# Performance work log

Hardware: AMD Instinct MI355X
Metric: run time of the kernel (lower is better)

The kernel has to match this reference:

```python
import jax, jax.numpy as jnp
import numpy as np

B = 16384
S0, S1 = 7, 7
NB, NC = 2, 20
WC, WN = 5.0, 0.5  # weight_coord, weight_noobject
D = NB * 5 + NC  # 30


def setup_inputs() -> dict:
    key = jax.random.key(0)
    k1, k2, k3, k4 = jax.random.split(key, 4)
    predication = jax.random.normal(k1, (B, S0 * S1 * D), dtype=jnp.float32)
    grid = jax.random.randint(k2, (B, S0, S1), 0, 2, dtype=jnp.int32)
    tbox = jax.random.uniform(k3, (B, S0, S1, 4), dtype=jnp.float32)
    # keep target w,h strictly positive (real boxes), offsets in [0,1)
    tbox = tbox.at[..., 2:].set(0.05 + 0.9 * tbox[..., 2:])
    tcls = jax.random.randint(k4, (B, S0, S1), 0, NC, dtype=jnp.int32)
    return {"predication": predication, "grid": grid, "tbox": tbox, "tcls": tcls}


def _yolo_loss(predication, grid, tbox, tcls):
    pred = predication.reshape(B, S0, S1, D)
    conf = jax.nn.sigmoid(pred[..., :NB])                                  # (B,S0,S1,NB)
    pb = jax.nn.sigmoid(pred[..., NB:5 * NB]).reshape(B, S0, S1, NB, 4)    # (B,S0,S1,NB,4)
    cls = jax.nn.softmax(pred[..., 5 * NB:], axis=-1)                      # (B,S0,S1,NC)

    # cell coordinates: x = column index, y = row index (matches the [1,0] swap in torch code)
    xg = jnp.arange(S1, dtype=pred.dtype)[None, None, :]   # (1,1,S1)
    yg = jnp.arange(S0, dtype=pred.dtype)[None, :, None]   # (1,S0,1)

    tox, toy, tw, th = tbox[..., 0], tbox[..., 1], tbox[..., 2], tbox[..., 3]
    tcx = (xg + tox) / S0
    tcy = (yg + toy) / S1

    pcx = (xg[..., None] + pb[..., 0]) / S0   # (B,S0,S1,NB)
    pcy = (yg[..., None] + pb[..., 1]) / S1
    pw, ph = pb[..., 2], pb[..., 3]

    # IOU of each predicted box vs the cell's target box (same formula as _calc_iou)
    tb_ = jnp.minimum(tcx[..., None] + tw[..., None] / 2, pcx + pw / 2) - \
          jnp.maximum(tcx[..., None] - tw[..., None] / 2, pcx - pw / 2)
    lr_ = jnp.minimum(tcy[..., None] + th[..., None] / 2, pcy + ph / 2) - \
          jnp.maximum(tcy[..., None] - th[..., None] / 2, pcy - ph / 2)
    inter = jnp.where((tb_ < 0) | (lr_ < 0), 0.0, tb_ * lr_)
    iou = inter / ((tw * th)[..., None] + pw * ph - inter)                 # (B,S0,S1,NB)

    # best predictor chosen on detached IOUs (original uses pred_boxes.detach())
    best = jnp.argmax(jax.lax.stop_gradient(iou), axis=-1)                 # (B,S0,S1)

    take = lambda a: jnp.take_along_axis(a, best[..., None], axis=-1)[..., 0]
    iou_b = take(iou)          # attached IOU re-used in confidence loss
    conf_b = take(conf)
    pbb = jnp.take_along_axis(pb, best[..., None, None], axis=3)[..., 0, :]  # (B,S0,S1,4)

    cls_t = jnp.take_along_axis(cls, tcls[..., None], axis=-1)[..., 0]

    coord = (pbb[..., 0] - tox) ** 2 + (pbb[..., 1] - toy) ** 2 \
          + (jnp.sqrt(pbb[..., 2]) - jnp.sqrt(tw)) ** 2 \
          + (jnp.sqrt(pbb[..., 3]) - jnp.sqrt(th)) ** 2

    obj_loss = WC * coord + (conf_b - iou_b) ** 2 + (1.0 - cls_t) ** 2     # (B,S0,S1)
    noobj_loss = WN * jnp.sum(conf ** 2, axis=-1)                          # (B,S0,S1)

    objm = (grid == 1).astype(pred.dtype)
    total = jnp.sum(objm * obj_loss + (1.0 - objm) * noobj_loss)
    return total / B


def reference(predication, grid, tbox, tcls):
    return _yolo_loss(predication, grid, tbox, tcls)
```

## Files before the change

### kernel.cpp

```cpp
#include <hip/hip_runtime.h>
#include <math.h>

namespace {

constexpr int kB    = 16384;
constexpr int kS0   = 7;
constexpr int kS1   = 7;
constexpr int kD    = 30;
constexpr int kCells = kB * kS0 * kS1;
constexpr int TPB   = 256;
constexpr int NBLK  = kCells / TPB;
constexpr int NSLOT = 64;
constexpr float kInv7 = 1.0f / 7.0f;
constexpr float kWC = 5.0f;
constexpr float kWN = 0.5f;

__device__ __forceinline__ float sigm(float x) {
    return 1.0f / (1.0f + __expf(-x));
}

__global__ void __launch_bounds__(TPB, 4) yolo_loss_kernel(
    const float* __restrict__ pred,
    const int*   __restrict__ grid,
    const float* __restrict__ tbox,
    const int*   __restrict__ tcls,
    float* __restrict__ partials)
{
    __shared__ float sp[TPB * kD];
    __shared__ float wsum[TPB / 64];

    const int tid   = threadIdx.x;
    const int cell0 = blockIdx.x * TPB;
    const int cell  = cell0 + tid;
    const int wave  = tid >> 6;
    const int lane  = tid & 63;

    const float4* __restrict__ g4 =
        reinterpret_cast<const float4*>(pred + (size_t)cell0 * kD);
    float4* s4 = reinterpret_cast<float4*>(sp);
    const int etid = 1792 + (tid & 127);

    float4 r[8];
    #pragma unroll
    for (int k = 0; k < 7; ++k) r[k] = g4[tid + 256 * k];
    r[7] = g4[etid];

    const float4 tb4 = reinterpret_cast<const float4*>(tbox)[cell];
    const int g  = grid[cell];
    const int tc = tcls[cell];

    __builtin_amdgcn_sched_barrier(0);

    #pragma unroll
    for (int k = 0; k < 7; ++k) s4[tid + 256 * k] = r[k];
    s4[etid] = r[7];
    __syncthreads();

    const int cj = cell % kS1;
    const int ci = (cell / kS1) % kS0;

    float f[kD];
    {
        const float2* p2 = reinterpret_cast<const float2*>(sp + tid * kD);
        #pragma unroll
        for (int q = 0; q < kD / 2; ++q) {
            float2 t = p2[q];
            f[2 * q]     = t.x;
            f[2 * q + 1] = t.y;
        }
    }

    const float tox = tb4.x, toy = tb4.y, tw = tb4.z, th = tb4.w;

    const float conf0 = sigm(f[0]);
    const float conf1 = sigm(f[1]);
    float pbx[2], pby[2], pbw[2], pbh[2];
    #pragma unroll
    for (int k = 0; k < 2; ++k) {
        pbx[k] = sigm(f[2 + 4 * k + 0]);
        pby[k] = sigm(f[2 + 4 * k + 1]);
        pbw[k] = sigm(f[2 + 4 * k + 2]);
        pbh[k] = sigm(f[2 + 4 * k + 3]);
    }

    float cmax = f[10];
    #pragma unroll
    for (int q = 11; q < 30; ++q) cmax = fmaxf(cmax, f[q]);
    float csum = 0.0f, et = 0.0f;
    #pragma unroll
    for (int q = 0; q < 20; ++q) {
        const float e = __expf(f[10 + q] - cmax);
        csum += e;
        et = (q == tc) ? e : et;
    }
    const float cls_t = et / csum;

    const float x = (float)cj, y = (float)ci;
    const float tcx = (x + tox) * kInv7;
    const float tcy = (y + toy) * kInv7;
    const float thw = tw * 0.5f, thh = th * 0.5f;
    const float tarea = tw * th;

    float iou[2];
    #pragma unroll
    for (int k = 0; k < 2; ++k) {
        const float pcx = (x + pbx[k]) * kInv7;
        const float pcy = (y + pby[k]) * kInv7;
        const float pw = pbw[k], ph = pbh[k];
        const float tb_ = fminf(tcx + thw, pcx + pw * 0.5f) - fmaxf(tcx - thw, pcx - pw * 0.5f);
        const float lr_ = fminf(tcy + thh, pcy + ph * 0.5f) - fmaxf(tcy - thh, pcy - ph * 0.5f);
        float inter = tb_ * lr_;
        inter = (tb_ < 0.0f || lr_ < 0.0f) ? 0.0f : inter;
        iou[k] = inter / (tarea + pw * ph - inter);
    }

    const bool b1 = (iou[1] > iou[0]);
    const float bx = b1 ? pbx[1] : pbx[0];
    const float by = b1 ? pby[1] : pby[0];
    const float bw = b1 ? pbw[1] : pbw[0];
    const float bh = b1 ? pbh[1] : pbh[0];
    const float conf_b = b1 ? conf1 : conf0;
    const float iou_b  = b1 ? iou[1] : iou[0];

    const float dx = bx - tox;
    const float dy = by - toy;
    const float dw = sqrtf(bw) - sqrtf(tw);
    const float dh = sqrtf(bh) - sqrtf(th);
    const float coord = dx * dx + dy * dy + dw * dw + dh * dh;
    const float d1 = conf_b - iou_b;
    const float d2 = 1.0f - cls_t;
    const float obj   = kWC * coord + d1 * d1 + d2 * d2;
    const float noobj = kWN * (conf0 * conf0 + conf1 * conf1);

    float v = (g == 1) ? obj : noobj;

    #pragma unroll
    for (int off = 32; off > 0; off >>= 1) v += __shfl_down(v, off, 64);
    if (lane == 0) wsum[wave] = v;
    __syncthreads();
    if (tid == 0) {
        atomicAdd(&partials[blockIdx.x & (NSLOT - 1)],
                  wsum[0] + wsum[1] + wsum[2] + wsum[3]);
    }
}

__global__ void finish_kernel(const float* __restrict__ partials,
                              float* __restrict__ out)
{
    float v = partials[threadIdx.x];
    #pragma unroll
    for (int off = 32; off > 0; off >>= 1) v += __shfl_down(v, off, 64);
    if (threadIdx.x == 0) out[0] = v * (1.0f / kB);
}

}

extern "C" void kernel_launch(void* const* d_in, const int* in_sizes, int n_in,
                              void* d_out, int out_size, void* d_ws, size_t ws_size,
                              hipStream_t stream) {
    const float* pred = (const float*)d_in[0];
    const int*   grid = (const int*)d_in[1];
    const float* tbox = (const float*)d_in[2];
    const int*   tcls = (const int*)d_in[3];
    float* out      = (float*)d_out;
    float* partials = (float*)d_ws;

    hipMemsetAsync(partials, 0, NSLOT * sizeof(float), stream);
    yolo_loss_kernel<<<NBLK, TPB, 0, stream>>>(pred, grid, tbox, tcls, partials);
    finish_kernel<<<1, 64, 0, stream>>>(partials, out);
}
```

Measured before the change: 160.4 us.

## Drop memset and atomics, use fast reciprocals, skip softmax max-subtraction

Each block now writes its partial sum to its own slot, so the memset launch and the atomics go away; the finish kernel then reduces all per-block partials with 256 threads. Divisions are replaced by the hardware reciprocal, and the softmax max-subtraction is removed. A scheduling barrier is added after the shared-memory loads. Dropping the max-subtraction risks exp overflow on large logits, and the reciprocal lowers precision. The finish kernel now has to read many partials serially per thread.

```diff
diff --git a/kernel.cpp b/kernel.cpp
--- a/kernel.cpp
+++ b/kernel.cpp
@@ -10,13 +10,16 @@
 constexpr int kCells = kB * kS0 * kS1;
 constexpr int TPB   = 256;
 constexpr int NBLK  = kCells / TPB;
-constexpr int NSLOT = 64;
 constexpr float kInv7 = 1.0f / 7.0f;
 constexpr float kWC = 5.0f;
 constexpr float kWN = 0.5f;
 
+__device__ __forceinline__ float frcp(float x) {
+    return __builtin_amdgcn_rcpf(x);
+}
+
 __device__ __forceinline__ float sigm(float x) {
-    return 1.0f / (1.0f + __expf(-x));
+    return frcp(1.0f + __expf(-x));
 }
 
 __global__ void __launch_bounds__(TPB, 4) yolo_loss_kernel(
@@ -68,6 +71,7 @@
             f[2 * q]     = t.x;
             f[2 * q + 1] = t.y;
         }
+        __builtin_amdgcn_sched_barrier(0);
     }
 
     const float tox = tb4.x, toy = tb4.y, tw = tb4.z, th = tb4.w;
@@ -83,17 +87,14 @@
         pbh[k] = sigm(f[2 + 4 * k + 3]);
     }
 
-    float cmax = f[10];
-    #pragma unroll
-    for (int q = 11; q < 30; ++q) cmax = fmaxf(cmax, f[q]);
     float csum = 0.0f, et = 0.0f;
     #pragma unroll
     for (int q = 0; q < 20; ++q) {
-        const float e = __expf(f[10 + q] - cmax);
+        const float e = __expf(f[10 + q]);
         csum += e;
         et = (q == tc) ? e : et;
     }
-    const float cls_t = et / csum;
+    const float cls_t = et * frcp(csum);
 
     const float x = (float)cj, y = (float)ci;
     const float tcx = (x + tox) * kInv7;
@@ -111,7 +112,7 @@
         const float lr_ = fminf(tcy + thh, pcy + ph * 0.5f) - fmaxf(tcy - thh, pcy - ph * 0.5f);
         float inter = tb_ * lr_;
         inter = (tb_ < 0.0f || lr_ < 0.0f) ? 0.0f : inter;
-        iou[k] = inter / (tarea + pw * ph - inter);
+        iou[k] = inter * frcp(tarea + pw * ph - inter);
     }
 
     const bool b1 = (iou[1] > iou[0]);
@@ -139,18 +140,22 @@
     if (lane == 0) wsum[wave] = v;
     __syncthreads();
     if (tid == 0) {
-        atomicAdd(&partials[blockIdx.x & (NSLOT - 1)],
-                  wsum[0] + wsum[1] + wsum[2] + wsum[3]);
+        partials[blockIdx.x] = wsum[0] + wsum[1] + wsum[2] + wsum[3];
     }
 }
 
-__global__ void finish_kernel(const float* __restrict__ partials,
-                              float* __restrict__ out)
+__global__ void __launch_bounds__(256) finish_kernel(
+    const float* __restrict__ partials, float* __restrict__ out)
 {
-    float v = partials[threadIdx.x];
+    __shared__ float wsum[4];
+    const int tid = threadIdx.x;
+    float v = 0.0f;
+    for (int i = tid; i < NBLK; i += 256) v += partials[i];
     #pragma unroll
     for (int off = 32; off > 0; off >>= 1) v += __shfl_down(v, off, 64);
-    if (threadIdx.x == 0) out[0] = v * (1.0f / kB);
+    if ((tid & 63) == 0) wsum[tid >> 6] = v;
+    __syncthreads();
+    if (tid == 0) out[0] = (wsum[0] + wsum[1] + wsum[2] + wsum[3]) * (1.0f / kB);
 }
 
 }
@@ -165,7 +170,6 @@
     float* out      = (float*)d_out;
     float* partials = (float*)d_ws;
 
-    hipMemsetAsync(partials, 0, NSLOT * sizeof(float), stream);
     yolo_loss_kernel<<<NBLK, TPB, 0, stream>>>(pred, grid, tbox, tcls, partials);
-    finish_kernel<<<1, 64, 0, stream>>>(partials, out);
+    finish_kernel<<<1, 256, 0, stream>>>(partials, out);
 }
```

Result: no change. 161.0 us (+0.4%).
